# Performance work log

Hardware: AMD Instinct MI355X
Metric: run time of the kernel (lower is better)

Reference implementation:

```python
import jax, jax.numpy as jnp
import numpy as np

B, Q, D_MODEL, H, D_HEAD, PAGE, N_PAGES = 8, 1024, 2048, 16, 128, 256, 8


def setup_inputs() -> dict:
    key = jax.random.key(0)
    ks = jax.random.split(key, 6)
    hidden_states = jax.random.normal(ks[0], (B, Q, D_MODEL), jnp.float32) * 0.02
    W_attn = jax.random.normal(ks[1], (D_MODEL, 3 * D_MODEL), jnp.float32) * 0.02
    b_attn = jnp.zeros((3 * D_MODEL,), jnp.float32)
    W_proj = jax.random.normal(ks[2], (D_MODEL, D_MODEL), jnp.float32) * 0.02
    b_proj = jnp.zeros((D_MODEL,), jnp.float32)
    k_pages = jax.random.normal(ks[3], (N_PAGES, B, H, PAGE, D_HEAD), jnp.float32)
    v_pages = jax.random.normal(ks[4], (N_PAGES, B, H, PAGE, D_HEAD), jnp.float32)
    # every cached page fully valid: (start=0, length=PAGE)
    page_pos = jnp.broadcast_to(jnp.array([0, PAGE], jnp.int32), (N_PAGES, B, 2))
    # current chunk: starts at end of cache, length = q_len
    input_pos = jnp.broadcast_to(jnp.array([N_PAGES * PAGE, Q], jnp.int32), (B, 2))
    return {
        "hidden_states": hidden_states,
        "W_attn": W_attn, "b_attn": b_attn,
        "W_proj": W_proj, "b_proj": b_proj,
        "k_pages": k_pages, "v_pages": v_pages,
        "page_pos": page_pos, "input_pos": input_pos,
    }


def reference(hidden_states, W_attn, b_attn, W_proj, b_proj,
              k_pages, v_pages, page_pos, input_pos):
    dtype = hidden_states.dtype
    NEG = jnp.finfo(dtype).min
    b, q_len, d_model = hidden_states.shape
    n_pages, _, num_heads, page_size, d_head = k_pages.shape
    scale = 1.0 / d_head ** 0.5

    # qkv projection (GPT2 c_attn)
    qkv = hidden_states @ W_attn + b_attn
    q, k_curr, v_curr = jnp.split(qkv, 3, axis=-1)

    def split_heads(x):  # [b, q, d_model] -> [b, h, q, d_head]
        return x.reshape(b, q_len, num_heads, d_head).transpose(0, 2, 1, 3)

    q = split_heads(q)
    k_curr = split_heads(k_curr)
    v_curr = split_heads(v_curr)

    # online softmax state
    m0 = jnp.full((b, num_heads, q_len, 1), NEG, dtype)
    l0 = jnp.zeros((b, num_heads, q_len, 1), dtype)
    acc0 = jnp.zeros((b, num_heads, q_len, d_head), dtype)

    kv_idx = jnp.arange(page_size)

    def page_step(carry, page):
        m, l, acc = carry
        k_p, v_p, pos = page  # [b,h,p,d], [b,h,p,d], [b,2]
        start, length = pos[:, 0], pos[:, 1]
        valid = (kv_idx[None, :] >= start[:, None]) & \
                (kv_idx[None, :] < (start + length)[:, None])  # [b, p]
        s = jnp.einsum('bhqd,bhpd->bhqp', q, k_p) * scale
        s = jnp.where(valid[:, None, None, :], s, NEG)
        m_p = s.max(axis=-1, keepdims=True)
        m_new = jnp.maximum(m, m_p)
        alpha = jnp.exp(m - m_new)
        e = jnp.exp(s - m_new)
        acc = alpha * acc + jnp.einsum('bhqp,bhpd->bhqd', e, v_p)
        l = alpha * l + e.sum(axis=-1, keepdims=True)
        return (m_new, l, acc), None

    (m, l, acc), _ = jax.lax.scan(page_step, (m0, l0, acc0),
                                  (k_pages, v_pages, page_pos))

    # final pass over current chunk: aligned start = 0, length from input_pos
    length = input_pos[:, 1]
    q_idx = jnp.arange(q_len)
    valid = q_idx[None, :] < length[:, None]                     # [b, q]
    causal = jnp.tril(jnp.ones((q_len, q_len), bool))            # keep lower tri
    s = jnp.einsum('bhqd,bhkd->bhqk', q, k_curr) * scale
    keep = valid[:, None, None, :] & causal[None, None, :, :]
    s = jnp.where(keep, s, NEG)
    m_p = s.max(axis=-1, keepdims=True)
    m_new = jnp.maximum(m, m_p)
    alpha = jnp.exp(m - m_new)
    e = jnp.exp(s - m_new)
    acc = alpha * acc + jnp.einsum('bhqk,bhkd->bhqd', e, v_curr)
    l = alpha * l + e.sum(axis=-1, keepdims=True)

    context = acc / jnp.maximum(l, 1e-9)
    context = context.transpose(0, 2, 1, 3).reshape(b, q_len, d_model)
    out = context @ W_proj + b_proj  # resid_dropout is identity in eval
    return out
```

## Files before the change

kernel.cpp:

```cpp
#include <hip/hip_runtime.h>

typedef __bf16 bf16;
typedef __bf16 bf16x8 __attribute__((ext_vector_type(8)));
typedef __bf16 bf16x4 __attribute__((ext_vector_type(4)));
typedef float f32x4 __attribute__((ext_vector_type(4)));
typedef unsigned short u16x4 __attribute__((ext_vector_type(4)));
typedef __attribute__((address_space(3))) const void as3_void;

#define GLOAD16(G,L) __builtin_amdgcn_global_load_lds((__attribute__((address_space(1))) const void*)(G), (__attribute__((address_space(3))) void*)(L), 16, 0, 0)

__global__ void k_cvt_bf16(const float* __restrict__ src, bf16* __restrict__ dst, int n4){
  int i = blockIdx.x*256 + threadIdx.x;
  if (i < n4){
    float4 v = reinterpret_cast<const float4*>(src)[i];
    bf16x4 o; o[0]=(bf16)v.x; o[1]=(bf16)v.y; o[2]=(bf16)v.z; o[3]=(bf16)v.w;
    reinterpret_cast<bf16x4*>(dst)[i] = o;
  }
}

__global__ void k_transpose_cvt(const float* __restrict__ src, bf16* __restrict__ dst, int K, int N){
  __shared__ float tile[32][33];
  int n0 = blockIdx.x*32, k0 = blockIdx.y*32;
  int tx = threadIdx.x & 31, ty = threadIdx.x >> 5;
  #pragma unroll
  for (int i=0;i<32;i+=8)
    tile[ty+i][tx] = src[(size_t)(k0+ty+i)*N + n0+tx];
  __syncthreads();
  #pragma unroll
  for (int i=0;i<32;i+=8)
    dst[(size_t)(n0+ty+i)*K + k0+tx] = (bf16)tile[tx][ty+i];
}

template<int EPI>
__global__ __launch_bounds__(512,2) void k_gemm8(
    const bf16* __restrict__ A, const bf16* __restrict__ Bt,
    const float* __restrict__ bias, int N, int K,
    bf16* __restrict__ q_out, bf16* __restrict__ k_out, bf16* __restrict__ v_out,
    float* __restrict__ c_out)
{
  __shared__ bf16 S[2][4][8192];
  const int t = threadIdx.x, w = t>>6, l = t&63, g = l>>4, c = l&15;
  const int wm = w>>2, wn = w&3;
  const int nb = N>>8;
  const int cpx = gridDim.x>>3;
  const int swz = (blockIdx.x&7)*cpx + (blockIdx.x>>3);
  const int m0 = (swz/nb)<<8, n0 = (swz%nb)<<8;
  const int NK = K>>6;
  const unsigned xorv = (unsigned)((l&7)<<4);

  const int r0 = t>>3;
  const int col0 = ((t&7) ^ (r0&7))<<3;

  auto stageA = [&](int kt2){
    #pragma unroll
    for (int hh=0; hh<2; ++hh){
      const bf16* sp = A + (size_t)(m0 + hh*128)*K + (kt2<<6);
      char* dp = (char*)&S[kt2&1][hh][0];
      GLOAD16(sp + (size_t)r0*K + col0,      dp + t*16);
      GLOAD16(sp + (size_t)(r0+64)*K + col0, dp + (t+512)*16);
    }
  };
  auto stageB = [&](int kt2){
    #pragma unroll
    for (int hh=0; hh<2; ++hh){
      const bf16* sp = Bt + (size_t)(n0 + hh*128)*K + (kt2<<6);
      char* dp = (char*)&S[kt2&1][2+hh][0];
      GLOAD16(sp + (size_t)r0*K + col0,      dp + t*16);
      GLOAD16(sp + (size_t)(r0+64)*K + col0, dp + (t+512)*16);
    }
  };

  f32x4 acc[8][4] = {};

  stageA(0); stageB(0);
  asm volatile("s_waitcnt vmcnt(0)" ::: "memory");
  __builtin_amdgcn_s_barrier();

  for (int kt=0; kt<NK; ++kt){
    const int bufc = kt&1;
    const char* Ab_ = (const char*)&S[bufc][wm][0];
    const char* Bb_ = (const char*)&S[bufc][2+(wn>>1)][0];
    const bool pre = (kt+1 < NK);
    bf16x8 af[4][2], bfr[2][2];

    auto lda = [&](int mh){
      #pragma unroll
      for (int mf=0; mf<4; ++mf)
        #pragma unroll
        for (int kk=0; kk<2; ++kk)
          af[mf][kk] = *reinterpret_cast<const bf16x8*>(Ab_ +
              (unsigned)((mh*64 + mf*16 + c)*128) + (((unsigned)(kk*64 + g*16)) ^ xorv));
    };
    auto ldb = [&](int nh){
      #pragma unroll
      for (int nf=0; nf<2; ++nf)
        #pragma unroll
        for (int kk=0; kk<2; ++kk)
          bfr[nf][kk] = *reinterpret_cast<const bf16x8*>(Bb_ +
              (unsigned)(((wn&1)*64 + nh*32 + nf*16 + c)*128) + (((unsigned)(kk*64 + g*16)) ^ xorv));
    };
    auto cluster = [&](int mh, int nh){
      __builtin_amdgcn_s_barrier();
      asm volatile("s_waitcnt lgkmcnt(0)" ::: "memory");
      __builtin_amdgcn_sched_barrier(0);
      __builtin_amdgcn_s_setprio(1);
      #pragma unroll
      for (int mf=0; mf<4; ++mf)
        #pragma unroll
        for (int nf=0; nf<2; ++nf)
          #pragma unroll
          for (int kk=0; kk<2; ++kk)
            acc[mh*4+mf][nh*2+nf] =
              __builtin_amdgcn_mfma_f32_16x16x32_bf16(af[mf][kk], bfr[nf][kk], acc[mh*4+mf][nh*2+nf], 0,0,0);
      __builtin_amdgcn_s_setprio(0);
    };

    lda(0); ldb(0);
    if (pre) stageA(kt+1);
    cluster(0,0);
    __builtin_amdgcn_s_barrier();
    ldb(1);
    if (pre) stageB(kt+1);
    cluster(0,1);
    __builtin_amdgcn_s_barrier();
    lda(1);
    cluster(1,1);
    __builtin_amdgcn_s_barrier();
    ldb(0);
    cluster(1,0);
    asm volatile("s_waitcnt vmcnt(0)" ::: "memory");
    __builtin_amdgcn_s_barrier();
  }

  if constexpr (EPI==0){
    #pragma unroll
    for (int NF=0; NF<4; ++NF){
      const int col = n0 + wn*64 + NF*16 + c;
      const int sec = col>>11; const int rem = col&2047;
      const int hhd = rem>>7;  const int dd = rem&127;
      bf16* dst = (sec==0) ? q_out : ((sec==1) ? k_out : v_out);
      const float bv = bias[col];
      const float qs = (sec==0) ? 0.12751743f : 1.0f;
      #pragma unroll
      for (int MF=0; MF<8; ++MF)
        #pragma unroll
        for (int ri=0; ri<4; ++ri){
          const int row = m0 + wm*128 + MF*16 + (g<<2) + ri;
          const int bb = row>>10, qp = row&1023;
          dst[(((size_t)(bb*16+hhd)*1024 + qp)<<7) + dd] = (bf16)((acc[MF][NF][ri] + bv)*qs);
        }
    }
  } else {
    #pragma unroll
    for (int NF=0; NF<4; ++NF){
      const int col = n0 + wn*64 + NF*16 + c;
      const float bv = bias[col];
      #pragma unroll
      for (int MF=0; MF<8; ++MF)
        #pragma unroll
        for (int ri=0; ri<4; ++ri){
          const int row = m0 + wm*128 + MF*16 + (g<<2) + ri;
          c_out[(size_t)row*N + col] = acc[MF][NF][ri] + bv;
        }
    }
  }
}

__global__ __launch_bounds__(512) __attribute__((amdgpu_waves_per_eu(4,4))) void k_attn(
    const bf16* __restrict__ qb, const bf16* __restrict__ kb, const bf16* __restrict__ vb,
    const bf16* __restrict__ kpb, const bf16* __restrict__ vpb,
    const int* __restrict__ page_pos, const int* __restrict__ input_pos,
    bf16* __restrict__ ctx)
{
  __shared__ bf16 Ks[2*64*128];
  __shared__ bf16 Vs[2*64*128];
  const int t = threadIdx.x, w = t>>6, l = t&63, g = l>>4, c = l&15;
  const int bid = blockIdx.x;
  const int wg = (bid&7)*128 + (bid>>3);
  const int qt = wg & 7, h = (wg>>3)&15, b = wg>>7;
  const int q0w = (qt<<7) + (w<<4);
  const size_t bh = (size_t)(b*16 + h);

  const bf16* qptr = qb + (bh<<17);
  bf16x8 qf[4];
  #pragma unroll
  for (int kc=0;kc<4;kc++)
    qf[kc] = *reinterpret_cast<const bf16x8*>(qptr + ((size_t)(q0w + c)<<7) + kc*32 + (g<<3));

  int kOff[2], vOff[2];
  #pragma unroll
  for (int j=0;j<2;j++){
    const int slot = t + (j<<9);
    {
      const int a = slot<<4; const int r = a>>8; const int co = (a&255) ^ ((r&7)<<4);
      kOff[j] = (r<<7) + (co>>1);
    }
    {
      const int s_ = slot;
      const int p  = ((s_>>6)<<2) | ((s_>>1)&3);
      const int d0 = (((s_>>3)&7)<<4) | ((s_&1)<<3);
      const int pp = (p&32) | ((p&4)<<2) | (((p>>3)&3)<<2) | (p&3);
      vOff[j] = (pp<<7) + d0;
    }
  }
  const bf16* kcb = kb + (bh<<17);
  const bf16* vcb = vb + (bh<<17);
  const int len_b = input_pos[b*2+1];
  const int NT = 32 + ((qt+1)<<1);

  f32x4 o[8] = {};
  float mrow = -1e38f;
  float lsum = 0.f;

  auto tsrc = [&](int T, const bf16*& ks, const bf16*& vs_){
    if (T < 32){
      size_t pb = ((((size_t)(T>>2)<<3) + (size_t)b)*16 + (size_t)h) << 15;
      size_t off = (size_t)(T&3)<<13;
      ks = kpb + pb + off; vs_ = vpb + pb + off;
    } else {
      int kt = T-32; ks = kcb + ((size_t)kt<<13); vs_ = vcb + ((size_t)kt<<13);
    }
  };
  auto stage = [&](int T, int buf){
    const bf16 *ks, *vs_; tsrc(T, ks, vs_);
    char* kd = (char*)Ks + (buf<<14) + (w<<10);
    char* vd = (char*)Vs + (buf<<14) + (w<<10);
    #pragma unroll
    for (int j=0;j<2;j++){
      GLOAD16(ks  + kOff[j], kd + (j<<13));
      GLOAD16(vs_ + vOff[j], vd + (j<<13));
    }
  };

  auto process = [&](int buf, int lo, int hi, bool masked, bool causal, int ktg){
    const char* Kb = (const char*)Ks + (buf<<14);
    const char* Vb = (const char*)Vs + (buf<<14);
    f32x4 s[4] = {};
    #pragma unroll
    for (int kc=0;kc<4;kc++){
      bf16x8 kf[4];
      #pragma unroll
      for (int cb=0;cb<4;cb++){
        const int krow = (cb<<4) + c;
        unsigned a = (unsigned)((krow<<8) + (kc<<6) + (g<<4)); a ^= (unsigned)((krow&7)<<4);
        kf[cb] = *reinterpret_cast<const bf16x8*>(Kb + a);
      }
      __builtin_amdgcn_s_setprio(1);
      #pragma unroll
      for (int cb=0;cb<4;cb++)
        s[cb] = __builtin_amdgcn_mfma_f32_16x16x32_bf16(kf[cb], qf[kc], s[cb], 0,0,0);
      __builtin_amdgcn_s_setprio(0);
    }
    if (masked){
      #pragma unroll
      for (int cb=0;cb<4;cb++)
        #pragma unroll
        for (int ri=0;ri<4;ri++){
          const int kvl = (cb<<4) + (g<<2) + ri;
          bool ok = (kvl >= lo) && (kvl < hi);
          if (causal) ok = ok && ((ktg + kvl) <= (q0w + c));
          s[cb][ri] = ok ? s[cb][ri] : -3e38f;
        }
    }
    {
      float mx = -3e38f;
      #pragma unroll
      for (int cb=0;cb<4;cb++)
        #pragma unroll
        for (int ri=0;ri<4;ri++) mx = fmaxf(mx, s[cb][ri]);
      mx = fmaxf(mx, __shfl_xor(mx, 16, 64));
      mx = fmaxf(mx, __shfl_xor(mx, 32, 64));
      const int defer = __all(mx - mrow <= 11.5f);
      if (!defer){
        const float mn = fmaxf(mrow, mx);
        const float al = exp2f(mrow - mn);
        mrow = mn;
        lsum *= al;
        #pragma unroll
        for (int ri=0;ri<4;ri++){
          const float av = __shfl(al, (l&48) | ((g<<2)+ri), 64);
          #pragma unroll
          for (int dcb=0;dcb<8;dcb++) o[dcb][ri] *= av;
        }
      }
      float ps = 0.f;
      #pragma unroll
      for (int cb=0;cb<4;cb++)
        #pragma unroll
        for (int ri=0;ri<4;ri++){
          const float e = exp2f(s[cb][ri] - mrow);
          s[cb][ri] = e; ps += e;
        }
      lsum += ps;
    }
    #pragma unroll
    for (int kc=0;kc<2;kc++){
      u16x4 vr0[8], vr1[8];
      #pragma unroll
      for (int dcb=0;dcb<8;dcb++){
        const unsigned sub = ((unsigned)((((kc<<3) + (g<<1))<<3) + dcb)<<7) + ((unsigned)c<<3);
        as3_void* pl = (as3_void*)(Vb + sub);
        asm volatile("ds_read_b64_tr_b16 %0, %2 offset:0\n\t"
                     "ds_read_b64_tr_b16 %1, %2 offset:1024"
                     : "=&v"(vr0[dcb]), "=&v"(vr1[dcb]) : "v"(pl) : "memory");
      }
      bf16x8 pav;
      #pragma unroll
      for (int e=0;e<8;e++)
        pav[e] = (bf16)s[(kc<<1)+(e>>2)][e&3];
      asm volatile("s_waitcnt lgkmcnt(0)" ::: "memory");
      __builtin_amdgcn_sched_barrier(0);
      __builtin_amdgcn_s_setprio(1);
      #pragma unroll
      for (int dcb=0;dcb<8;dcb++){
        union { unsigned short us[8]; bf16x8 v; } uu;
        #pragma unroll
        for (int i=0;i<4;i++){ uu.us[i]=vr0[dcb][i]; uu.us[4+i]=vr1[dcb][i]; }
        o[dcb] = __builtin_amdgcn_mfma_f32_16x16x32_bf16(pav, uu.v, o[dcb], 0,0,0);
      }
      __builtin_amdgcn_s_setprio(0);
    }
  };

  int buf = 0;
  stage(0, 0);
  asm volatile("s_waitcnt vmcnt(0)" ::: "memory");
  __syncthreads();
  for (int T=0; T<NT; ++T){
    if (T+1 < NT) stage(T+1, buf^1);
    int lo=0, hi=64, ktg=0; bool causal=false, masked=false, skip=false;
    if (T < 32){
      const int pg = T>>2, to = T&3;
      const int start = page_pos[(pg*8+b)*2], plen = page_pos[(pg*8+b)*2+1];
      lo = start - (to<<6); hi = start + plen - (to<<6); if (hi>64) hi=64;
      masked = (lo > 0) || (hi < 64);
      skip = (hi <= 0) || (lo >= 64);
    } else {
      const int kt = T-32; ktg = kt<<6;
      hi = len_b - ktg; if (hi>64) hi=64;
      skip = (ktg > q0w + 15) || (hi <= 0);
      causal = (ktg + 63 > q0w);
      masked = causal || (hi < 64);
    }
    if (!skip) process(buf, lo, hi, masked, causal, ktg);
    asm volatile("s_waitcnt vmcnt(0)" ::: "memory");
    __syncthreads();
    buf ^= 1;
  }

  {
    float tl = lsum;
    tl += __shfl_xor(tl, 16, 64);
    tl += __shfl_xor(tl, 32, 64);
    const float inv = 1.f / fmaxf(tl, 1e-9f);
    #pragma unroll
    for (int ri=0;ri<4;ri++){
      const float iv = __shfl(inv, (l&48) | ((g<<2)+ri), 64);
      const int q = q0w + (g<<2) + ri;
      #pragma unroll
      for (int dcb=0;dcb<8;dcb++)
        ctx[(((size_t)(b<<10) + q)<<11) + (h<<7) + (dcb<<4) + c] = (bf16)(o[dcb][ri]*iv);
    }
  }
}

extern "C" void kernel_launch(void* const* d_in, const int* in_sizes, int n_in,
                              void* d_out, int out_size, void* d_ws, size_t ws_size,
                              hipStream_t stream)
{
  const float* hidden  = (const float*)d_in[0];
  const float* W_attn  = (const float*)d_in[1];
  const float* b_attn  = (const float*)d_in[2];
  const float* W_proj  = (const float*)d_in[3];
  const float* b_proj  = (const float*)d_in[4];
  const float* k_pages = (const float*)d_in[5];
  const float* v_pages = (const float*)d_in[6];
  const int*   page_pos  = (const int*)d_in[7];
  const int*   input_pos = (const int*)d_in[8];
  float* out = (float*)d_out;
  char* ws = (char*)d_ws;
  bf16* A1  = (bf16*)(ws);
  bf16* Wt1 = (bf16*)(ws + 33554432);
  bf16* Wt2 = (bf16*)(ws + 58720256);
  bf16* qb  = (bf16*)(ws + 67108864);
  bf16* kb  = (bf16*)(ws + 100663296);
  bf16* vb  = (bf16*)(ws + 134217728);
  bf16* kpb = (bf16*)(ws + 167772160);
  bf16* vpb = (bf16*)(ws + 234881024);
  bf16* ctx = A1;

  k_cvt_bf16<<<16384, 256, 0, stream>>>(hidden, A1, 4194304);
  k_cvt_bf16<<<32768, 256, 0, stream>>>(k_pages, kpb, 8388608);
  k_cvt_bf16<<<32768, 256, 0, stream>>>(v_pages, vpb, 8388608);
  k_transpose_cvt<<<dim3(192,64), 256, 0, stream>>>(W_attn, Wt1, 2048, 6144);
  k_transpose_cvt<<<dim3(64,64),  256, 0, stream>>>(W_proj, Wt2, 2048, 2048);
  k_gemm8<0><<<768, 512, 0, stream>>>(A1, Wt1, b_attn, 6144, 2048, qb, kb, vb, nullptr);
  k_attn<<<1024, 512, 0, stream>>>(qb, kb, vb, kpb, vpb, page_pos, input_pos, ctx);
  k_gemm8<1><<<256, 512, 0, stream>>>(ctx, Wt2, b_proj, 2048, 2048, nullptr, nullptr, nullptr, out);
}
```

Before: 727.3 us.

## Split K/V staging: double-buffer K, single-buffer V with phased barriers

The attention loop now double-buffers only the K tile and keeps a single V buffer. The next V tile is loaded after the current P·V step and overlaps with the next QK^T and softmax. Finer vmcnt waits and separate barriers gate the QK and PV phases independently, and the V LDS reads are split into two halves to cut live registers. This reduces LDS footprint and register pressure, at the cost of extra barriers and a shorter window for hiding V load latency.

```diff
diff --git a/kernel.cpp b/kernel.cpp
--- a/kernel.cpp
+++ b/kernel.cpp
@@ -173,7 +173,7 @@
     bf16* __restrict__ ctx)
 {
   __shared__ bf16 Ks[2*64*128];
-  __shared__ bf16 Vs[2*64*128];
+  __shared__ bf16 Vs[64*128];
   const int t = threadIdx.x, w = t>>6, l = t&63, g = l>>4, c = l&15;
   const int bid = blockIdx.x;
   const int wg = (bid&7)*128 + (bid>>3);
@@ -221,113 +221,24 @@
       int kt = T-32; ks = kcb + ((size_t)kt<<13); vs_ = vcb + ((size_t)kt<<13);
     }
   };
-  auto stage = [&](int T, int buf){
+  auto stage_K = [&](int T){
     const bf16 *ks, *vs_; tsrc(T, ks, vs_);
-    char* kd = (char*)Ks + (buf<<14) + (w<<10);
-    char* vd = (char*)Vs + (buf<<14) + (w<<10);
-    #pragma unroll
-    for (int j=0;j<2;j++){
-      GLOAD16(ks  + kOff[j], kd + (j<<13));
-      GLOAD16(vs_ + vOff[j], vd + (j<<13));
-    }
+    char* kd = (char*)Ks + ((T&1)<<14) + (w<<10);
+    GLOAD16(ks + kOff[0], kd);
+    GLOAD16(ks + kOff[1], kd + (1<<13));
   };
-
-  auto process = [&](int buf, int lo, int hi, bool masked, bool causal, int ktg){
-    const char* Kb = (const char*)Ks + (buf<<14);
-    const char* Vb = (const char*)Vs + (buf<<14);
-    f32x4 s[4] = {};
-    #pragma unroll
-    for (int kc=0;kc<4;kc++){
-      bf16x8 kf[4];
-      #pragma unroll
-      for (int cb=0;cb<4;cb++){
-        const int krow = (cb<<4) + c;
-        unsigned a = (unsigned)((krow<<8) + (kc<<6) + (g<<4)); a ^= (unsigned)((krow&7)<<4);
-        kf[cb] = *reinterpret_cast<const bf16x8*>(Kb + a);
-      }
-      __builtin_amdgcn_s_setprio(1);
-      #pragma unroll
-      for (int cb=0;cb<4;cb++)
-        s[cb] = __builtin_amdgcn_mfma_f32_16x16x32_bf16(kf[cb], qf[kc], s[cb], 0,0,0);
-      __builtin_amdgcn_s_setprio(0);
-    }
-    if (masked){
-      #pragma unroll
-      for (int cb=0;cb<4;cb++)
-        #pragma unroll
-        for (int ri=0;ri<4;ri++){
-          const int kvl = (cb<<4) + (g<<2) + ri;
-          bool ok = (kvl >= lo) && (kvl < hi);
-          if (causal) ok = ok && ((ktg + kvl) <= (q0w + c));
-          s[cb][ri] = ok ? s[cb][ri] : -3e38f;
-        }
-    }
-    {
-      float mx = -3e38f;
-      #pragma unroll
-      for (int cb=0;cb<4;cb++)
-        #pragma unroll
-        for (int ri=0;ri<4;ri++) mx = fmaxf(mx, s[cb][ri]);
-      mx = fmaxf(mx, __shfl_xor(mx, 16, 64));
-      mx = fmaxf(mx, __shfl_xor(mx, 32, 64));
-      const int defer = __all(mx - mrow <= 11.5f);
-      if (!defer){
-        const float mn = fmaxf(mrow, mx);
-        const float al = exp2f(mrow - mn);
-        mrow = mn;
-        lsum *= al;
-        #pragma unroll
-        for (int ri=0;ri<4;ri++){
-          const float av = __shfl(al, (l&48) | ((g<<2)+ri), 64);
-          #pragma unroll
-          for (int dcb=0;dcb<8;dcb++) o[dcb][ri] *= av;
-        }
-      }
-      float ps = 0.f;
-      #pragma unroll
-      for (int cb=0;cb<4;cb++)
-        #pragma unroll
-        for (int ri=0;ri<4;ri++){
-          const float e = exp2f(s[cb][ri] - mrow);
-          s[cb][ri] = e; ps += e;
-        }
-      lsum += ps;
-    }
-    #pragma unroll
-    for (int kc=0;kc<2;kc++){
-      u16x4 vr0[8], vr1[8];
-      #pragma unroll
-      for (int dcb=0;dcb<8;dcb++){
-        const unsigned sub = ((unsigned)((((kc<<3) + (g<<1))<<3) + dcb)<<7) + ((unsigned)c<<3);
-        as3_void* pl = (as3_void*)(Vb + sub);
-        asm volatile("ds_read_b64_tr_b16 %0, %2 offset:0\n\t"
-                     "ds_read_b64_tr_b16 %1, %2 offset:1024"
-                     : "=&v"(vr0[dcb]), "=&v"(vr1[dcb]) : "v"(pl) : "memory");
-      }
-      bf16x8 pav;
-      #pragma unroll
-      for (int e=0;e<8;e++)
-        pav[e] = (bf16)s[(kc<<1)+(e>>2)][e&3];
-      asm volatile("s_waitcnt lgkmcnt(0)" ::: "memory");
-      __builtin_amdgcn_sched_barrier(0);
-      __builtin_amdgcn_s_setprio(1);
-      #pragma unroll
-      for (int dcb=0;dcb<8;dcb++){
-        union { unsigned short us[8]; bf16x8 v; } uu;
-        #pragma unroll
-        for (int i=0;i<4;i++){ uu.us[i]=vr0[dcb][i]; uu.us[4+i]=vr1[dcb][i]; }
-        o[dcb] = __builtin_amdgcn_mfma_f32_16x16x32_bf16(pav, uu.v, o[dcb], 0,0,0);
-      }
-      __builtin_amdgcn_s_setprio(0);
-    }
+  auto stage_V = [&](int T){
+    const bf16 *ks, *vs_; tsrc(T, ks, vs_);
+    char* vd = (char*)Vs + (w<<10);
+    GLOAD16(vs_ + vOff[0], vd);
+    GLOAD16(vs_ + vOff[1], vd + (1<<13));
   };
 
-  int buf = 0;
-  stage(0, 0);
-  asm volatile("s_waitcnt vmcnt(0)" ::: "memory");
-  __syncthreads();
+  stage_K(0);
+  stage_V(0);
+
   for (int T=0; T<NT; ++T){
-    if (T+1 < NT) stage(T+1, buf^1);
+    const bool pre = (T+1 < NT);
     int lo=0, hi=64, ktg=0; bool causal=false, masked=false, skip=false;
     if (T < 32){
       const int pg = T>>2, to = T&3;
@@ -342,10 +253,113 @@
       causal = (ktg + 63 > q0w);
       masked = causal || (hi < 64);
     }
-    if (!skip) process(buf, lo, hi, masked, causal, ktg);
-    asm volatile("s_waitcnt vmcnt(0)" ::: "memory");
-    __syncthreads();
-    buf ^= 1;
+
+    if (pre) stage_K(T+1);
+    if (pre) { asm volatile("s_waitcnt vmcnt(4)" ::: "memory"); }
+    else     { asm volatile("s_waitcnt vmcnt(2)" ::: "memory"); }
+    __builtin_amdgcn_s_barrier();
+
+    f32x4 s[4] = {};
+    if (!skip){
+      const char* Kb = (const char*)Ks + ((T&1)<<14);
+      #pragma unroll
+      for (int kc=0;kc<4;kc++){
+        bf16x8 kf[4];
+        #pragma unroll
+        for (int cb=0;cb<4;cb++){
+          const int krow = (cb<<4) + c;
+          unsigned a = (unsigned)((krow<<8) + (kc<<6) + (g<<4)); a ^= (unsigned)((krow&7)<<4);
+          kf[cb] = *reinterpret_cast<const bf16x8*>(Kb + a);
+        }
+        __builtin_amdgcn_s_setprio(1);
+        #pragma unroll
+        for (int cb=0;cb<4;cb++)
+          s[cb] = __builtin_amdgcn_mfma_f32_16x16x32_bf16(kf[cb], qf[kc], s[cb], 0,0,0);
+        __builtin_amdgcn_s_setprio(0);
+      }
+      if (masked){
+        #pragma unroll
+        for (int cb=0;cb<4;cb++)
+          #pragma unroll
+          for (int ri=0;ri<4;ri++){
+            const int kvl = (cb<<4) + (g<<2) + ri;
+            bool ok = (kvl >= lo) && (kvl < hi);
+            if (causal) ok = ok && ((ktg + kvl) <= (q0w + c));
+            s[cb][ri] = ok ? s[cb][ri] : -3e38f;
+          }
+      }
+      float mx = -3e38f;
+      #pragma unroll
+      for (int cb=0;cb<4;cb++)
+        #pragma unroll
+        for (int ri=0;ri<4;ri++) mx = fmaxf(mx, s[cb][ri]);
+      mx = fmaxf(mx, __shfl_xor(mx, 16, 64));
+      mx = fmaxf(mx, __shfl_xor(mx, 32, 64));
+      const int defer = __all(mx - mrow <= 11.5f);
+      if (!defer){
+        const float mn = fmaxf(mrow, mx);
+        const float al = exp2f(mrow - mn);
+        mrow = mn;
+        lsum *= al;
+        #pragma unroll
+        for (int ri=0;ri<4;ri++){
+          const float av = __shfl(al, (l&48) | ((g<<2)+ri), 64);
+          #pragma unroll
+          for (int dcb=0;dcb<8;dcb++) o[dcb][ri] *= av;
+        }
+      }
+      float ps = 0.f;
+      #pragma unroll
+      for (int cb=0;cb<4;cb++)
+        #pragma unroll
+        for (int ri=0;ri<4;ri++){
+          const float e = exp2f(s[cb][ri] - mrow);
+          s[cb][ri] = e; ps += e;
+        }
+      lsum += ps;
+    }
+
+    if (pre) { asm volatile("s_waitcnt vmcnt(2)" ::: "memory"); }
+    else     { asm volatile("s_waitcnt vmcnt(0)" ::: "memory"); }
+    __builtin_amdgcn_s_barrier();
+
+    if (!skip){
+      const char* Vb = (const char*)Vs;
+      #pragma unroll
+      for (int kc=0;kc<2;kc++){
+        bf16x8 pav;
+        #pragma unroll
+        for (int e=0;e<8;e++)
+          pav[e] = (bf16)s[(kc<<1)+(e>>2)][e&3];
+        #pragma unroll
+        for (int hb=0;hb<2;hb++){
+          u16x4 vr0[4], vr1[4];
+          #pragma unroll
+          for (int d4=0;d4<4;d4++){
+            const int dcb = (hb<<2) + d4;
+            const unsigned sub = ((unsigned)((((kc<<3) + (g<<1))<<3) + dcb)<<7) + ((unsigned)c<<3);
+            as3_void* pl = (as3_void*)(Vb + sub);
+            asm volatile("ds_read_b64_tr_b16 %0, %2 offset:0\n\t"
+                         "ds_read_b64_tr_b16 %1, %2 offset:1024"
+                         : "=&v"(vr0[d4]), "=&v"(vr1[d4]) : "v"(pl) : "memory");
+          }
+          asm volatile("s_waitcnt lgkmcnt(0)" ::: "memory");
+          __builtin_amdgcn_sched_barrier(0);
+          __builtin_amdgcn_s_setprio(1);
+          #pragma unroll
+          for (int d4=0;d4<4;d4++){
+            union { unsigned short us[8]; bf16x8 v; } uu;
+            #pragma unroll
+            for (int i=0;i<4;i++){ uu.us[i]=vr0[d4][i]; uu.us[4+i]=vr1[d4][i]; }
+            o[(hb<<2)+d4] = __builtin_amdgcn_mfma_f32_16x16x32_bf16(pav, uu.v, o[(hb<<2)+d4], 0,0,0);
+          }
+          __builtin_amdgcn_s_setprio(0);
+        }
+      }
+    }
+
+    __builtin_amdgcn_s_barrier();
+    if (pre) stage_V(T+1);
   }
 
   {
```

Measured after the change: 883.6 us. +21.5%, slower.
